# Performance work log

Measured on AMD Instinct MI355X. Metric: run time of the kernel, lower is better.

The kernel has to match this reference:

```python
import jax, jax.numpy as jnp
import numpy as np
from jax import lax

H_SP, W_SP = 32, 8   # idx == 0
NUM_HEADS = 2
DIM = 64
SCALE = (DIM // NUM_HEADS) ** -0.5


def conv1x1(x, w, b):
    # x: [B,C,H,W], w: [O,C,1,1], b: [O]
    return jnp.einsum('bchw,oc->bohw', x, w[:, :, 0, 0]) + b[None, :, None, None]


def dwconv5(x, w, b):
    # depthwise 5x5, pad 2. w: [C,1,5,5]
    y = lax.conv_general_dilated(
        x, w, window_strides=(1, 1), padding=[(2, 2), (2, 2)],
        dimension_numbers=('NCHW', 'OIHW', 'NCHW'),
        feature_group_count=x.shape[1])
    return y + b[None, :, None, None]


def im2cswin(x):
    # [B,C,H,W] -> [B*nH*nW, heads, H_SP*W_SP, C//heads]
    B, C, H, W = x.shape
    x = x.reshape(B, C, H // H_SP, H_SP, W // W_SP, W_SP)
    x = x.transpose(0, 2, 4, 3, 5, 1).reshape(-1, H_SP * W_SP, NUM_HEADS, C // NUM_HEADS)
    return x.transpose(0, 2, 1, 3)


def windows2img(xw, H, W):
    # [B', H_SP*W_SP, C] -> [B, C, H, W]
    B = xw.shape[0] // ((H // H_SP) * (W // W_SP))
    x = xw.reshape(B, H // H_SP, W // W_SP, H_SP, W_SP, -1)
    return x.transpose(0, 5, 1, 3, 2, 4).reshape(B, -1, H, W)


def setup_inputs() -> dict:
    key = jax.random.key(0)
    ks = jax.random.split(key, 8)
    B, C, H, W = 4, DIM, 256, 256
    s = 0.02
    return {
        'x': jax.random.normal(ks[0], (B, C, H, W), dtype=jnp.float32),
        'qk_w': jax.random.normal(ks[1], (2 * C, C, 1, 1), dtype=jnp.float32) * s,
        'qk_b': jnp.zeros((2 * C,), jnp.float32),
        'q5_w': jax.random.normal(ks[2], (C, 1, 5, 5), dtype=jnp.float32) * s,
        'q5_b': jnp.zeros((C,), jnp.float32),
        'k5_w': jax.random.normal(ks[3], (C, 1, 5, 5), dtype=jnp.float32) * s,
        'k5_b': jnp.zeros((C,), jnp.float32),
        'v_w': jax.random.normal(ks[4], (C, C, 1, 1), dtype=jnp.float32) * s,
        'v_b': jnp.zeros((C,), jnp.float32),
        'lepe_w': jax.random.normal(ks[5], (C, 1, 5, 5), dtype=jnp.float32) * s,
        'lepe_b': jnp.zeros((C,), jnp.float32),
    }


def reference(x, qk_w, qk_b, q5_w, q5_b, k5_w, k5_b, v_w, v_b, lepe_w, lepe_b):
    B, C, H, W = x.shape
    pad_r = (W_SP - W % W_SP) % W_SP
    pad_b = (H_SP - H % H_SP) % H_SP
    xp = jnp.pad(x, ((0, 0), (0, 0), (0, pad_b), (0, pad_r)))
    Hp, Wp = xp.shape[2], xp.shape[3]
    # shift_size == 0 -> no roll
    qk = conv1x1(xp, qk_w, qk_b)
    q, k = jnp.split(qk, 2, axis=1)
    v = conv1x1(xp, v_w, v_b)
    lepe = dwconv5(v, lepe_w, lepe_b)
    qw = im2cswin(dwconv5(q, q5_w, q5_b) + lepe)   # [nw, h, N, d]
    kw = im2cswin(dwconv5(k, k5_w, k5_b) + lepe)
    vw = im2cswin(v)
    attn = jnp.einsum('whnd,whmd->whnm', qw * SCALE, kw)
    attn = jax.nn.softmax(attn, axis=-1)
    out = jnp.einsum('whnm,whmd->whnd', attn, vw)
    out = out.transpose(0, 2, 1, 3).reshape(-1, H_SP * W_SP, C)
    out = windows2img(out, Hp, Wp) + lepe
    if pad_r or pad_b:
        out = out[:, :, :H, :W]
    return out
```

## Files before the change

kernel.cpp:

```cpp
#include <hip/hip_runtime.h>


typedef unsigned short u16;
typedef short s16x8 __attribute__((ext_vector_type(8)));
typedef float f32x4 __attribute__((ext_vector_type(4)));

#define MFMA16(a, b, c) __builtin_amdgcn_mfma_f32_16x16x32_bf16((a), (b), (c), 0, 0, 0)

#define SCALE_F 0.17677669529663687f
#define LOG2E_F 1.4426950408889634f

#if __has_builtin(__builtin_amdgcn_exp2f)
#define EXP2F(x) __builtin_amdgcn_exp2f(x)
#else
#define EXP2F(x) exp2f(x)
#endif

#if __has_builtin(__builtin_amdgcn_rcpf)
#define RCPF(x) __builtin_amdgcn_rcpf(x)
#else
#define RCPF(x) (1.f / (x))
#endif

__device__ __forceinline__ u16 f2bf(float f) {
  unsigned u = __float_as_uint(f);
  return (u16)((u + 0x7FFFu + ((u >> 16) & 1u)) >> 16);
}
__device__ __forceinline__ float bf2f(u16 h) {
  return __uint_as_float(((unsigned)h) << 16);
}
__device__ __forceinline__ unsigned pk_rne(float lo, float hi) {
  unsigned ul = __float_as_uint(lo), uh = __float_as_uint(hi);
  ul += 0x7FFFu + ((ul >> 16) & 1u);
  uh += 0x7FFFu + ((uh >> 16) & 1u);
  return (ul >> 16) | (uh & 0xFFFF0000u);
}

__global__ __launch_bounds__(256, 4) void k1_conv1x1(
    const float* __restrict__ x, const float* __restrict__ qk_w,
    const float* __restrict__ qk_b, const float* __restrict__ v_w,
    const float* __restrict__ v_b, u16* __restrict__ qkv) {
  __shared__ u16 Wl[12288];
  __shared__ float Bl[192];
  int t = threadIdx.x;
  for (int i = t; i < 12288; i += 256) {
    int oc = i >> 6, ic = i & 63;
    float wv_ = (oc < 128) ? qk_w[i] : v_w[i - 8192];
    Wl[(oc << 6) | (ic ^ ((oc & 7) << 3))] = f2bf(wv_);
  }
  if (t < 192) Bl[t] = (t < 128) ? qk_b[t] : v_b[t - 128];
  __syncthreads();

  int lane = t & 63, wv = t >> 6;
  int col = lane & 15, g = lane >> 4;
  int p0 = blockIdx.x * 64 + wv * 16;
  int b = p0 >> 16, pix0 = p0 & 65535;

  const float* xb = x + (size_t)b * 4194304 + pix0 + col;
  s16x8 bfrag[2];
#pragma unroll
  for (int kk = 0; kk < 2; ++kk) {
#pragma unroll
    for (int j = 0; j < 8; ++j) {
      int ic = kk * 32 + g * 8 + j;
      bfrag[kk][j] = (short)f2bf(xb[(size_t)ic << 16]);
    }
  }

  f32x4 acc[12];
#pragma unroll
  for (int mt = 0; mt < 12; ++mt) acc[mt] = 0.f;
#pragma unroll
  for (int mt = 0; mt < 12; ++mt) {
    int oc = mt * 16 + col;
    int swz = (oc & 7) << 3;
#pragma unroll
    for (int kk = 0; kk < 2; ++kk) {
      s16x8 af = *(const s16x8*)&Wl[(oc << 6) | ((kk * 32 + g * 8) ^ swz)];
      acc[mt] = MFMA16(af, bfrag[kk], acc[mt]);
    }
  }

  u16* ob = qkv + (size_t)b * 12582912 + pix0 + col;
#pragma unroll
  for (int mt = 0; mt < 12; ++mt) {
#pragma unroll
    for (int r = 0; r < 4; ++r) {
      int oc = mt * 16 + g * 4 + r;
      ob[(size_t)oc << 16] = f2bf(acc[mt][r] + Bl[oc]);
    }
  }
}


__device__ __forceinline__ int qt_off(int tok, int d) {
  return (tok << 5) + (d ^ (((tok >> 2) & 3) << 3));
}
__device__ __forceinline__ int vt_off(int d, int tok) {
  int swz = (((d & 7) ^ ((tok >> 6) & 3)) << 3);
  return (d << 8) + ((tok & ~7) ^ swz) + (tok & 7);
}

__global__ __launch_bounds__(512, 4) void k23_fused(
    const u16* __restrict__ qkv, const float* __restrict__ q5_w,
    const float* __restrict__ q5_b, const float* __restrict__ k5_w,
    const float* __restrict__ k5_b, const float* __restrict__ lepe_w,
    const float* __restrict__ lepe_b, float* __restrict__ out) {
  __shared__ u16 SM[38912];
  u16* QT = SM;
  u16* KT = SM + 8192;
  u16* VT = SM + 16384;
  u16* LT = SM + 24576;
  u16* HS = SM + 32768;
  u16* WLb = SM + 36224;
  float* BLf = (float*)(SM + 38720);

  int raw = blockIdx.x;
  int bid = (raw & 7) * 256 + (raw >> 3);
  int head = bid & 1, wj = (bid >> 1) & 31, wi = (bid >> 6) & 7, b = bid >> 9;
  int h0 = wi * 32, w0 = wj * 8;

  int t = threadIdx.x;
  int wv = t >> 6, lane = t & 63;
  int dl = lane & 7, tq = lane >> 3;
  const size_t bbase = (size_t)b * 12582912;

  for (int i = t; i < 2400; i += 512) {
    int ts = i / 800, rem = i - ts * 800, ch = rem / 25, j = rem - ch * 25;
    const float* srcw = (ts == 0 ? lepe_w : ts == 1 ? q5_w : k5_w);
    WLb[ts * 832 + ch * 26 + j] = f2bf(srcw[(head * 32 + ch) * 25 + j]);
  }
  if (t < 96) {
    int ts = t >> 5, ch = t & 31;
    BLf[t] = (ts == 0 ? lepe_b : ts == 1 ? q5_b : k5_b)[head * 32 + ch];
  }

  unsigned fixOff[4], okm[4];
  int ldsOff[4];
  bool live[4];
#pragma unroll
  for (int it = 0; it < 4; ++it) {
    int ip = t + it * 512;
    live[it] = ip < 1728;
    int ipc = live[it] ? ip : 0;
    int ch = ipc / 216, rem = ipc - ch * 216;
    int hr = rem / 6, hc = rem - hr * 6;
    int gh = h0 - 2 + hr, gw = w0 - 2 + hc * 2;
    bool ok = live[it] & ((unsigned)gh < 256u) & ((unsigned)gw <= 254u);
    int hcl = gh < 0 ? 0 : (gh > 255 ? 255 : gh);
    int wcl = gw < 0 ? 0 : (gw > 254 ? 254 : gw);
    fixOff[it] = ((unsigned)ch << 16) + hcl * 256 + wcl;
    okm[it] = ok ? 0xffffffffu : 0u;
    ldsOff[it] = (ch * 36 + hr) * 12 + hc * 2;
  }

  unsigned cr[4];
  auto stage_ld = [&](int p) {
    int cg = p / 3, ts = p - cg * 3;
    int planeBase = (ts == 0 ? 128 : ts == 1 ? 0 : 64) + head * 32 + cg * 8;
    const u16* src = qkv + bbase + ((size_t)planeBase << 16);
#pragma unroll
    for (int it = 0; it < 4; ++it)
      if (live[it]) {
        unsigned v = *(const unsigned*)&src[fixOff[it]];
        cr[it] = v & okm[it];
      }
  };
  auto stage_st = [&]() {
#pragma unroll
    for (int it = 0; it < 4; ++it)
      if (live[it]) *(unsigned*)&HS[ldsOff[it]] = cr[it];
  };

  stage_ld(0);
  stage_st();
  __syncthreads();

  int row = wv * 4 + (tq >> 1), c0 = (tq & 1) * 4;
  int tok0 = wv * 32 + tq * 4;
  float lepA[4];

#pragma unroll 1
  for (int p = 0; p < 12; ++p) {
    if (p < 11) stage_ld(p + 1);
    int cg = p / 3, ts = p - cg * 3;
    int d = cg * 8 + dl;

    float wr[25];
    {
      const u16* wb = &WLb[ts * 832 + d * 26];
#pragma unroll
      for (int k2 = 0; k2 < 12; ++k2) {
        unsigned u = *(const unsigned*)&wb[k2 * 2];
        wr[2 * k2] = __uint_as_float(u << 16);
        wr[2 * k2 + 1] = __uint_as_float(u & 0xffff0000u);
      }
      wr[24] = bf2f(wb[24]);
    }
    float bias = BLf[ts * 32 + d];

    const u16* hb = &HS[(dl * 36 + row) * 12 + c0];
    float acc[4] = {bias, bias, bias, bias};
    float ctr[4];
#pragma unroll
    for (int i = 0; i < 5; ++i) {
      uint2 A = *(const uint2*)&hb[i * 12];
      uint2 Bv = *(const uint2*)&hb[i * 12 + 4];
      float px[8];
      px[0] = __uint_as_float(A.x << 16);
      px[1] = __uint_as_float(A.x & 0xffff0000u);
      px[2] = __uint_as_float(A.y << 16);
      px[3] = __uint_as_float(A.y & 0xffff0000u);
      px[4] = __uint_as_float(Bv.x << 16);
      px[5] = __uint_as_float(Bv.x & 0xffff0000u);
      px[6] = __uint_as_float(Bv.y << 16);
      px[7] = __uint_as_float(Bv.y & 0xffff0000u);
      if (ts == 0 && i == 2) {
#pragma unroll
        for (int j = 0; j < 4; ++j) ctr[j] = px[j + 2];
      }
#pragma unroll
      for (int jj = 0; jj < 5; ++jj) {
        float w5 = wr[i * 5 + jj];
#pragma unroll
        for (int j = 0; j < 4; ++j) acc[j] = fmaf(px[j + jj], w5, acc[j]);
      }
    }

    if (ts == 0) {
      uint2 ol;
      ol.x = pk_rne(acc[0], acc[1]);
      ol.y = pk_rne(acc[2], acc[3]);
      *(uint2*)&LT[vt_off(d, tok0)] = ol;
      unsigned pv01 = pk_rne(ctr[0], ctr[1]), pv23 = pk_rne(ctr[2], ctr[3]);
      int aa = tok0 >> 5, h2 = (tok0 >> 4) & 1, cc = tok0 & 15;
      int sb = aa * 32 + cc * 2 + h2;
      VT[vt_off(d, sb)] = (u16)pv01;
      VT[vt_off(d, sb + 2)] = (u16)(pv01 >> 16);
      VT[vt_off(d, sb + 4)] = (u16)pv23;
      VT[vt_off(d, sb + 6)] = (u16)(pv23 >> 16);
#pragma unroll
      for (int j = 0; j < 4; ++j) lepA[j] = acc[j];
    } else {
      u16* tile = (ts == 1) ? QT : KT;
      float o0 = acc[0] + lepA[0], o1 = acc[1] + lepA[1];
      float o2 = acc[2] + lepA[2], o3 = acc[3] + lepA[3];
      if (ts == 1) {
        o0 *= SCALE_F;
        o1 *= SCALE_F;
        o2 *= SCALE_F;
        o3 *= SCALE_F;
      }
      unsigned q01 = pk_rne(o0, o1), q23 = pk_rne(o2, o3);
      tile[qt_off(tok0, d)] = (u16)q01;
      tile[qt_off(tok0 + 1, d)] = (u16)(q01 >> 16);
      tile[qt_off(tok0 + 2, d)] = (u16)q23;
      tile[qt_off(tok0 + 3, d)] = (u16)(q23 >> 16);
    }
    __syncthreads();
    if (p < 11) {
      stage_st();
      __syncthreads();
    }
  }

  int col = lane & 15, g = lane >> 4;
  int rbase = wv * 32;

  s16x8 qa[2];
  float lepr[2][8];
#pragma unroll
  for (int mt = 0; mt < 2; ++mt) {
    int tok = rbase + mt * 16 + col;
    qa[mt] = *(const s16x8*)&QT[qt_off(tok, g * 8)];
#pragma unroll
    for (int dt = 0; dt < 2; ++dt)
#pragma unroll
      for (int r = 0; r < 4; ++r) {
        int d = dt * 16 + g * 4 + r;
        lepr[mt][dt * 4 + r] = bf2f(LT[vt_off(d, tok)]);
      }
  }
  __syncthreads();

  u16* Pw = (wv < 4) ? (SM + wv * 2048) : (SM + 24576 + (wv - 4) * 2048);
  float* ob = out + (((size_t)(b * 64 + head * 32)) << 16) + h0 * 256 + w0;

#pragma unroll 1
  for (int mt = 0; mt < 2; ++mt) {
    int row0 = rbase + mt * 16;
    f32x4 zero = 0.f;
    f32x4 sacc[16];
#pragma unroll
    for (int nt = 0; nt < 16; ++nt) {
      int tj = nt * 16 + col;
      s16x8 kb = *(const s16x8*)&KT[qt_off(tj, g * 8)];
      sacc[nt] = MFMA16(qa[mt], kb, zero);
    }
    float mx[4];
#pragma unroll
    for (int r = 0; r < 4; ++r) {
      float m = sacc[0][r];
#pragma unroll
      for (int nt = 1; nt < 15; nt += 2)
        m = fmaxf(m, fmaxf(sacc[nt][r], sacc[nt + 1][r]));
      m = fmaxf(m, sacc[15][r]);
#pragma unroll
      for (int s = 1; s < 16; s <<= 1) m = fmaxf(m, __shfl_xor(m, s));
      mx[r] = m;
    }
    float ssum[4];
#pragma unroll
    for (int r = 0; r < 4; ++r) {
      float cm = -mx[r] * LOG2E_F;
      float s0 = 0.f;
#pragma unroll
      for (int nt = 0; nt < 16; ++nt) {
        float pv = EXP2F(fmaf(sacc[nt][r], LOG2E_F, cm));
        sacc[nt][r] = pv;
        s0 += pv;
      }
#pragma unroll
      for (int s = 1; s < 16; s <<= 1) s0 += __shfl_xor(s0, s);
      ssum[r] = s0;
    }
    int srcl = (col >> 2) << 4;
    float t0 = __shfl(ssum[0], srcl);
    float t1 = __shfl(ssum[1], srcl);
    float t2 = __shfl(ssum[2], srcl);
    float t3 = __shfl(ssum[3], srcl);
    float sA = (col & 1) ? t1 : t0;
    float sB = (col & 1) ? t3 : t2;
    float inv = RCPF((col & 2) ? sB : sA);

    f32x4 oacc[2];
    oacc[0] = 0.f;
    oacc[1] = 0.f;
    unsigned* PwU = (unsigned*)Pw;
#pragma unroll
    for (int chunk = 0; chunk < 2; ++chunk) {
#pragma unroll
      for (int r = 0; r < 4; ++r) {
        int irow = g * 4 + r;
        int wb = irow * 64;
        int sw = (irow & 7) << 2;
#pragma unroll
        for (int al = 0; al < 4; ++al) {
          int nt = chunk * 8 + al * 2;
          PwU[wb + ((al * 16 + col) ^ sw)] =
              pk_rne(sacc[nt][r], sacc[nt + 1][r]);
        }
      }
#pragma unroll
      for (int ks = 0; ks < 4; ++ks) {
        int kcp = (ks * 16 + g * 4) ^ ((col & 7) << 2);
        s16x8 pb = *(const s16x8*)&PwU[col * 64 + kcp];
        int sig = chunk * 128 + ks * 32 + g * 8;
#pragma unroll
        for (int dt = 0; dt < 2; ++dt) {
          s16x8 va = *(const s16x8*)&VT[vt_off(dt * 16 + col, sig)];
          oacc[dt] = MFMA16(va, pb, oacc[dt]);
        }
      }
    }
    int tok = row0 + col;
#pragma unroll
    for (int dt = 0; dt < 2; ++dt) {
#pragma unroll
      for (int r = 0; r < 4; ++r) {
        int d = dt * 16 + g * 4 + r;
        float val = fmaf(oacc[dt][r], inv, lepr[mt][dt * 4 + r]);
        ob[((size_t)d << 16) + (tok >> 3) * 256 + (tok & 7)] = val;
      }
    }
  }
}

extern "C" void kernel_launch(void* const* d_in, const int* in_sizes, int n_in,
                              void* d_out, int out_size, void* d_ws,
                              size_t ws_size, hipStream_t stream) {
  const float* x = (const float*)d_in[0];
  const float* qk_w = (const float*)d_in[1];
  const float* qk_b = (const float*)d_in[2];
  const float* q5_w = (const float*)d_in[3];
  const float* q5_b = (const float*)d_in[4];
  const float* k5_w = (const float*)d_in[5];
  const float* k5_b = (const float*)d_in[6];
  const float* v_w = (const float*)d_in[7];
  const float* v_b = (const float*)d_in[8];
  const float* lepe_w = (const float*)d_in[9];
  const float* lepe_b = (const float*)d_in[10];
  float* out = (float*)d_out;

  if (ws_size < 100663296ull) return;
  u16* qkv = (u16*)d_ws;

  hipLaunchKernelGGL(k1_conv1x1, dim3(4096), dim3(256), 0, stream, x, qk_w,
                     qk_b, v_w, v_b, qkv);
  hipLaunchKernelGGL(k23_fused, dim3(2048), dim3(512), 0, stream, qkv, q5_w,
                     q5_b, k5_w, k5_b, lepe_w, lepe_b, out);
}
```

Baseline: 215.4 us.

## Use bf16 dot2 for depthwise 5x5 conv and pack LDS writes via lane shuffles

Pre-packs the 5x5 depthwise weights as paired bf16 words in shared memory and computes the conv with fdot2_f32_bf16 on packed pixel pairs, replacing scalar unpack-and-FMA work. The 12-step stage loop is unrolled into four channel groups with three specialised stages each. Q/K and V tile stores become 32-bit and 64-bit writes, with values exchanged between lanes through shuffles, instead of scattered 16-bit stores. The cost is extra shuffle traffic and a little more shared memory, plus small rounding differences from dot2 accumulation.

```diff
diff --git a/kernel.cpp b/kernel.cpp
--- a/kernel.cpp
+++ b/kernel.cpp
@@ -20,6 +20,18 @@
 #define RCPF(x) __builtin_amdgcn_rcpf(x)
 #else
 #define RCPF(x) (1.f / (x))
+#endif
+
+#if __has_builtin(__builtin_amdgcn_fdot2_f32_bf16)
+#define HAVE_DOT2 1
+typedef __bf16 bf16x2_t __attribute__((ext_vector_type(2)));
+__device__ __forceinline__ float dot2bf(unsigned a, unsigned b, float c) {
+  return __builtin_amdgcn_fdot2_f32_bf16(__builtin_bit_cast(bf16x2_t, a),
+                                         __builtin_bit_cast(bf16x2_t, b), c,
+                                         false);
+}
+#else
+#define HAVE_DOT2 0
 #endif
 
 __device__ __forceinline__ u16 f2bf(float f) {
@@ -101,19 +113,66 @@
   return (d << 8) + ((tok & ~7) ^ swz) + (tok & 7);
 }
 
+template <bool WANTC>
+__device__ __forceinline__ void conv25(const u16* hb, const unsigned* ww,
+                                       float* acc, unsigned& cA, unsigned& cB) {
+#pragma unroll
+  for (int i = 0; i < 5; ++i) {
+    uint2 A = *(const uint2*)&hb[i * 12];
+    uint2 Bv = *(const uint2*)&hb[i * 12 + 4];
+    if (WANTC && i == 2) {
+      cA = A.y;
+      cB = Bv.x;
+    }
+#if HAVE_DOT2
+    unsigned o1 = (A.x >> 16) | (A.y << 16);
+    unsigned o3 = (A.y >> 16) | (Bv.x << 16);
+    unsigned o5 = (Bv.x >> 16) | (Bv.y << 16);
+    unsigned o7 = (Bv.y >> 16) | (Bv.y << 16);
+    unsigned pr[8] = {A.x, o1, A.y, o3, Bv.x, o5, Bv.y, o7};
+#pragma unroll
+    for (int j = 0; j < 4; ++j) {
+      float a0 = dot2bf(pr[j], ww[i * 3], acc[j]);
+      a0 = dot2bf(pr[j + 2], ww[i * 3 + 1], a0);
+      acc[j] = dot2bf(pr[j + 4], ww[i * 3 + 2], a0);
+    }
+#else
+    float px[8];
+    px[0] = __uint_as_float(A.x << 16);
+    px[1] = __uint_as_float(A.x & 0xffff0000u);
+    px[2] = __uint_as_float(A.y << 16);
+    px[3] = __uint_as_float(A.y & 0xffff0000u);
+    px[4] = __uint_as_float(Bv.x << 16);
+    px[5] = __uint_as_float(Bv.x & 0xffff0000u);
+    px[6] = __uint_as_float(Bv.y << 16);
+    px[7] = __uint_as_float(Bv.y & 0xffff0000u);
+    float w5[5];
+    w5[0] = __uint_as_float(ww[i * 3] << 16);
+    w5[1] = __uint_as_float(ww[i * 3] & 0xffff0000u);
+    w5[2] = __uint_as_float(ww[i * 3 + 1] << 16);
+    w5[3] = __uint_as_float(ww[i * 3 + 1] & 0xffff0000u);
+    w5[4] = __uint_as_float(ww[i * 3 + 2] << 16);
+#pragma unroll
+    for (int jj = 0; jj < 5; ++jj)
+#pragma unroll
+      for (int j = 0; j < 4; ++j) acc[j] = fmaf(px[j + jj], w5[jj], acc[j]);
+#endif
+  }
+}
+
 __global__ __launch_bounds__(512, 4) void k23_fused(
     const u16* __restrict__ qkv, const float* __restrict__ q5_w,
     const float* __restrict__ q5_b, const float* __restrict__ k5_w,
     const float* __restrict__ k5_b, const float* __restrict__ lepe_w,
     const float* __restrict__ lepe_b, float* __restrict__ out) {
-  __shared__ u16 SM[38912];
+  __shared__ u16 SM[39488];
   u16* QT = SM;
   u16* KT = SM + 8192;
   u16* VT = SM + 16384;
   u16* LT = SM + 24576;
   u16* HS = SM + 32768;
-  u16* WLb = SM + 36224;
-  float* BLf = (float*)(SM + 38720);
+  unsigned* WLp = (unsigned*)(SM + 36224);
+  float* BLf = (float*)(SM + 39296);
 
   int raw = blockIdx.x;
   int bid = (raw & 7) * 256 + (raw >> 3);
@@ -125,10 +184,14 @@
   int dl = lane & 7, tq = lane >> 3;
   const size_t bbase = (size_t)b * 12582912;
 
-  for (int i = t; i < 2400; i += 512) {
-    int ts = i / 800, rem = i - ts * 800, ch = rem / 25, j = rem - ch * 25;
-    const float* srcw = (ts == 0 ? lepe_w : ts == 1 ? q5_w : k5_w);
-    WLb[ts * 832 + ch * 26 + j] = f2bf(srcw[(head * 32 + ch) * 25 + j]);
+  for (int i = t; i < 1440; i += 512) {
+    int ts = i / 480, rem = i - ts * 480, ch = rem / 15, rk = rem - ch * 15;
+    int r = rk / 3, k2 = rk - r * 3;
+    const float* srcw = (ts == 0 ? lepe_w : ts == 1 ? q5_w : k5_w) +
+                        (head * 32 + ch) * 25 + r * 5 + k2 * 2;
+    float lo = srcw[0];
+    float hi = (k2 < 2) ? srcw[1] : 0.f;
+    WLp[ts * 512 + ch * 16 + rk] = pk_rne(lo, hi);
   }
   if (t < 96) {
     int ts = t >> 5, ch = t & 31;
@@ -178,87 +241,89 @@
 
   int row = wv * 4 + (tq >> 1), c0 = (tq & 1) * 4;
   int tok0 = wv * 32 + tq * 4;
+  int hq = tq >> 2;
+  int sBv = wv * 32 + (tq & 3) * 8 + hq * 4;
+  int qjb = (dl & 1) ? 2 : 0;
+  const u16* hb = &HS[(dl * 36 + row) * 12 + c0];
   float lepA[4];
 
+  auto loadw = [&](int ts, int d, unsigned* ww) {
+    const uint4* wp = (const uint4*)(WLp + ts * 512 + d * 16);
+    uint4 a = wp[0], b4 = wp[1], c4 = wp[2], e4 = wp[3];
+    ww[0] = a.x; ww[1] = a.y; ww[2] = a.z; ww[3] = a.w;
+    ww[4] = b4.x; ww[5] = b4.y; ww[6] = b4.z; ww[7] = b4.w;
+    ww[8] = c4.x; ww[9] = c4.y; ww[10] = c4.z; ww[11] = c4.w;
+    ww[12] = e4.x; ww[13] = e4.y; ww[14] = e4.z;
+  };
+
+  auto do_qk = [&](const unsigned* ww, float bias, u16* tile, bool doScale,
+                   int d) {
+    float acc[4] = {bias, bias, bias, bias};
+    unsigned du0, du1;
+    conv25<false>(hb, ww, acc, du0, du1);
+    float o0 = acc[0] + lepA[0], o1 = acc[1] + lepA[1];
+    float o2 = acc[2] + lepA[2], o3 = acc[3] + lepA[3];
+    if (doScale) {
+      o0 *= SCALE_F;
+      o1 *= SCALE_F;
+      o2 *= SCALE_F;
+      o3 *= SCALE_F;
+    }
+    unsigned q01 = pk_rne(o0, o1), q23 = pk_rne(o2, o3);
+    unsigned sendq = (dl & 1) ? q01 : q23;
+    unsigned recvq = (unsigned)__shfl_xor((int)sendq, 1);
+    unsigned aQ = (dl & 1) ? recvq : q01;
+    unsigned bQ = (dl & 1) ? q23 : recvq;
+    unsigned wlo = (aQ & 0xffffu) | (bQ << 16);
+    unsigned whi = (aQ >> 16) | (bQ & 0xffff0000u);
+    int dp = d & ~1;
+    unsigned* tw = (unsigned*)tile;
+    int wq0 = ((tok0 + qjb) << 4) + ((dp ^ ((tq & 3) << 3)) >> 1);
+    tw[wq0] = wlo;
+    tw[wq0 + 16] = whi;
+  };
+
 #pragma unroll 1
-  for (int p = 0; p < 12; ++p) {
-    if (p < 11) stage_ld(p + 1);
-    int cg = p / 3, ts = p - cg * 3;
+  for (int cg = 0; cg < 4; ++cg) {
+    int p3 = cg * 3;
     int d = cg * 8 + dl;
-
-    float wr[25];
+    unsigned ww[16];
+    stage_ld(p3 + 1);
+    loadw(0, d, ww);
     {
-      const u16* wb = &WLb[ts * 832 + d * 26];
-#pragma unroll
-      for (int k2 = 0; k2 < 12; ++k2) {
-        unsigned u = *(const unsigned*)&wb[k2 * 2];
-        wr[2 * k2] = __uint_as_float(u << 16);
-        wr[2 * k2 + 1] = __uint_as_float(u & 0xffff0000u);
-      }
-      wr[24] = bf2f(wb[24]);
-    }
-    float bias = BLf[ts * 32 + d];
-
-    const u16* hb = &HS[(dl * 36 + row) * 12 + c0];
-    float acc[4] = {bias, bias, bias, bias};
-    float ctr[4];
-#pragma unroll
-    for (int i = 0; i < 5; ++i) {
-      uint2 A = *(const uint2*)&hb[i * 12];
-      uint2 Bv = *(const uint2*)&hb[i * 12 + 4];
-      float px[8];
-      px[0] = __uint_as_float(A.x << 16);
-      px[1] = __uint_as_float(A.x & 0xffff0000u);
-      px[2] = __uint_as_float(A.y << 16);
-      px[3] = __uint_as_float(A.y & 0xffff0000u);
-      px[4] = __uint_as_float(Bv.x << 16);
-      px[5] = __uint_as_float(Bv.x & 0xffff0000u);
-      px[6] = __uint_as_float(Bv.y << 16);
-      px[7] = __uint_as_float(Bv.y & 0xffff0000u);
-      if (ts == 0 && i == 2) {
-#pragma unroll
-        for (int j = 0; j < 4; ++j) ctr[j] = px[j + 2];
-      }
-#pragma unroll
-      for (int jj = 0; jj < 5; ++jj) {
-        float w5 = wr[i * 5 + jj];
-#pragma unroll
-        for (int j = 0; j < 4; ++j) acc[j] = fmaf(px[j + jj], w5, acc[j]);
-      }
-    }
-
-    if (ts == 0) {
+      float bias = BLf[d];
+      float acc[4] = {bias, bias, bias, bias};
+      unsigned cA, cB;
+      conv25<true>(hb, ww, acc, cA, cB);
       uint2 ol;
       ol.x = pk_rne(acc[0], acc[1]);
       ol.y = pk_rne(acc[2], acc[3]);
       *(uint2*)&LT[vt_off(d, tok0)] = ol;
-      unsigned pv01 = pk_rne(ctr[0], ctr[1]), pv23 = pk_rne(ctr[2], ctr[3]);
-      int aa = tok0 >> 5, h2 = (tok0 >> 4) & 1, cc = tok0 & 15;
-      int sb = aa * 32 + cc * 2 + h2;
-      VT[vt_off(d, sb)] = (u16)pv01;
-      VT[vt_off(d, sb + 2)] = (u16)(pv01 >> 16);
-      VT[vt_off(d, sb + 4)] = (u16)pv23;
-      VT[vt_off(d, sb + 6)] = (u16)(pv23 >> 16);
+      unsigned sendv = hq ? cA : cB;
+      unsigned recvv = (unsigned)__shfl_xor((int)sendv, 32);
+      unsigned aW = hq ? recvv : cA;
+      unsigned bW = hq ? cB : recvv;
+      uint2 ov;
+      ov.x = (aW & 0xffffu) | (bW << 16);
+      ov.y = (aW >> 16) | (bW & 0xffff0000u);
+      *(uint2*)&VT[vt_off(d, sBv)] = ov;
 #pragma unroll
       for (int j = 0; j < 4; ++j) lepA[j] = acc[j];
-    } else {
-      u16* tile = (ts == 1) ? QT : KT;
-      float o0 = acc[0] + lepA[0], o1 = acc[1] + lepA[1];
-      float o2 = acc[2] + lepA[2], o3 = acc[3] + lepA[3];
-      if (ts == 1) {
-        o0 *= SCALE_F;
-        o1 *= SCALE_F;
-        o2 *= SCALE_F;
-        o3 *= SCALE_F;
-      }
-      unsigned q01 = pk_rne(o0, o1), q23 = pk_rne(o2, o3);
-      tile[qt_off(tok0, d)] = (u16)q01;
-      tile[qt_off(tok0 + 1, d)] = (u16)(q01 >> 16);
-      tile[qt_off(tok0 + 2, d)] = (u16)q23;
-      tile[qt_off(tok0 + 3, d)] = (u16)(q23 >> 16);
     }
     __syncthreads();
-    if (p < 11) {
+    stage_st();
+    __syncthreads();
+    stage_ld(p3 + 2);
+    loadw(1, d, ww);
+    do_qk(ww, BLf[32 + d], QT, true, d);
+    __syncthreads();
+    stage_st();
+    __syncthreads();
+    if (cg < 3) stage_ld(p3 + 3);
+    loadw(2, d, ww);
+    do_qk(ww, BLf[64 + d], KT, false, d);
+    __syncthreads();
+    if (cg < 3) {
       stage_st();
       __syncthreads();
     }
```

Measured after the change: 213.2 us. No clear change (-1.0%).
